# Kernel tuning notes

Hardware: AMD Instinct MI355X
Metric: run time of the kernel (lower is better)

## Reference

```python
import jax, jax.numpy as jnp
import numpy as np

D_MODEL = 1024
D_FF = 4096
N_EXPERTS = 8
THRESHOLD = 0.8
EPS = 1e-6


def setup_inputs() -> dict:
    key = jax.random.key(0)
    ks = jax.random.split(key, 8)
    x = jax.random.normal(ks[0], (2, 1024, D_MODEL), jnp.float32)
    Wg = jax.random.normal(ks[1], (D_MODEL, N_EXPERTS), jnp.float32) * (D_MODEL ** -0.5)
    bg = jnp.zeros((N_EXPERTS,), jnp.float32)
    W1 = jax.random.normal(ks[2], (N_EXPERTS, D_MODEL, D_FF), jnp.float32) * (D_MODEL ** -0.5)
    b1 = jnp.zeros((N_EXPERTS, D_FF), jnp.float32)
    W3 = jax.random.normal(ks[3], (N_EXPERTS, D_MODEL, D_FF), jnp.float32) * (D_MODEL ** -0.5)
    b3 = jnp.zeros((N_EXPERTS, D_FF), jnp.float32)
    W2 = jax.random.normal(ks[4], (N_EXPERTS, D_FF, D_MODEL), jnp.float32) * (D_FF ** -0.5)
    b2 = jnp.zeros((N_EXPERTS, D_MODEL), jnp.float32)
    return {"x": x, "Wg": Wg, "bg": bg, "W1": W1, "b1": b1, "W3": W3, "b3": b3, "W2": W2, "b2": b2}


def _route(x, Wg, bg):
    # Dynamic-K (top-p) router
    logits = x @ Wg + bg                                  # [B,S,E]
    probs = jax.nn.softmax(logits, axis=-1)
    order = jnp.argsort(-probs, axis=-1)                  # descending sort indices
    sp = jnp.take_along_axis(probs, order, axis=-1)       # sorted probs
    shifted = jnp.cumsum(sp, axis=-1) - sp                # exclusive cumsum
    active = shifted < THRESHOLD
    active = active.at[..., 0].set(True)                  # always keep top-1
    ap = sp * active.astype(sp.dtype)
    aw = ap / (ap.sum(axis=-1, keepdims=True) + EPS)      # renormalized weights
    inv = jnp.argsort(order, axis=-1)                     # scatter == gather by inverse perm
    weights = jnp.take_along_axis(aw, inv, axis=-1)       # [B,S,E] in expert order
    return weights, probs, active.sum(axis=-1)


def reference(x, Wg, bg, W1, b1, W3, b3, W2, b2):
    B, S, D = x.shape
    E = W1.shape[0]
    weights, probs, active_count = _route(x, Wg, bg)
    xf = x.reshape(-1, D)                                 # [T,D]
    wf = weights.reshape(-1, E)                           # [T,E]
    # Dense grouped SwiGLU experts; zero routing weight zeroes the contribution,
    # matching the masked gather/scatter math of the original.
    h = jnp.einsum('td,edf->etf', xf, W1) + b1[:, None, :]
    g = jax.nn.silu(h) * (jnp.einsum('td,edf->etf', xf, W3) + b3[:, None, :])
    out_e = jnp.einsum('etf,efd->etd', g, W2) + b2[:, None, :]
    final = jnp.einsum('etd,te->td', out_e, wf).reshape(B, S, D)
    # auxiliary losses
    f_i = (wf > 0).astype(x.dtype).mean(axis=0)           # fraction of tokens per expert
    P_i = probs.reshape(-1, E).mean(axis=0)               # mean router prob per expert
    loss_balance = E * jnp.sum(f_i * P_i)
    loss_entropy = (-jnp.sum(probs * jnp.log(probs + EPS), axis=-1)).mean()
    return final, loss_balance, loss_entropy, active_count
```

## Files before the change

kernel.cpp:

```cpp
#include <hip/hip_runtime.h>
#include <hip/hip_bf16.h>
#include <math.h>

#define D_MODEL 1024
#define D_FF    4096
#define N_EXP   8
#define TOKENS  2048
#define THRESH  0.8f
#define EPS_R   1e-6f

#define FINAL_SIZE (TOKENS * D_MODEL)

typedef unsigned short ushort_t;
typedef __attribute__((ext_vector_type(4))) float f32x4;
typedef __attribute__((ext_vector_type(8))) short bf16x8;
typedef __attribute__((ext_vector_type(8))) unsigned short ushort8_t;

__device__ __forceinline__ unsigned short f2bf(float f) {
    unsigned u = __builtin_bit_cast(unsigned, f);
    unsigned r = (u + 0x7FFFu + ((u >> 16) & 1u)) >> 16;
    return (unsigned short)r;
}

template <typename T>
__device__ __forceinline__ void gload16(const T* gsrc, T* ldst) {
    __builtin_amdgcn_global_load_lds((const __attribute__((address_space(1))) unsigned int*)gsrc,
                                     (__attribute__((address_space(3))) unsigned int*)ldst,
                                     16, 0, 0);
}

__global__ __launch_bounds__(256) void convert_x_kernel(const float* __restrict__ x,
                                                        ushort_t* __restrict__ xbf) {
    int i = blockIdx.x * 256 + threadIdx.x;
    const float4 v = reinterpret_cast<const float4*>(x)[i];
    ushort4 o;
    o.x = f2bf(v.x); o.y = f2bf(v.y); o.z = f2bf(v.z); o.w = f2bf(v.w);
    reinterpret_cast<ushort4*>(xbf)[i] = o;
}

__global__ __launch_bounds__(256) void wconv_kernel(const float* __restrict__ in,
                                                    ushort_t* __restrict__ out,
                                                    int K, int N) {
    __shared__ float sT[32][65];
    const int e = blockIdx.z;
    const float* src = in + (size_t)e * K * N;
    ushort_t* dst = out + (size_t)e * K * N;
    const int k0 = blockIdx.y * 32, n0 = blockIdx.x * 64;
    const int t = threadIdx.x;
    {
        const int k = t >> 3;
        const int n4 = (t & 7) * 8;
        const float* s = src + (size_t)(k0 + k) * N + n0 + n4;
        float4 a = *reinterpret_cast<const float4*>(s);
        float4 b = *reinterpret_cast<const float4*>(s + 4);
        sT[k][n4 + 0] = a.x; sT[k][n4 + 1] = a.y; sT[k][n4 + 2] = a.z; sT[k][n4 + 3] = a.w;
        sT[k][n4 + 4] = b.x; sT[k][n4 + 5] = b.y; sT[k][n4 + 6] = b.z; sT[k][n4 + 7] = b.w;
    }
    __syncthreads();
    {
        const int n = t >> 2;
        const int kg = (t & 3) * 8;
        ushort8_t o;
#pragma unroll
        for (int j = 0; j < 8; ++j) o[j] = f2bf(sT[kg + j][n]);
        *reinterpret_cast<ushort8_t*>(dst + (size_t)(n0 + n) * K + k0 + kg) = o;
    }
}

__global__ __launch_bounds__(256) void router_kernel(const float* __restrict__ x,
                                                     const float* __restrict__ Wg,
                                                     const float* __restrict__ bg,
                                                     float* __restrict__ wts,
                                                     float* __restrict__ probs,
                                                     float* __restrict__ ent,
                                                     float* __restrict__ act_out)
{
    int wave = threadIdx.x >> 6;
    int lane = threadIdx.x & 63;
    int t = blockIdx.x * 4 + wave;

    float acc[8];
#pragma unroll
    for (int e = 0; e < 8; ++e) acc[e] = 0.f;

    const float* xrow = x + (size_t)t * D_MODEL;
    for (int d = lane; d < D_MODEL; d += 64) {
        float xv = xrow[d];
        const float4* wg = reinterpret_cast<const float4*>(Wg + (size_t)d * 8);
        float4 a = wg[0], b = wg[1];
        acc[0] += xv * a.x; acc[1] += xv * a.y; acc[2] += xv * a.z; acc[3] += xv * a.w;
        acc[4] += xv * b.x; acc[5] += xv * b.y; acc[6] += xv * b.z; acc[7] += xv * b.w;
    }
#pragma unroll
    for (int e = 0; e < 8; ++e) {
#pragma unroll
        for (int off = 32; off > 0; off >>= 1) acc[e] += __shfl_xor(acc[e], off);
    }

    if (lane == 0) {
        float l[8], p[8];
        float m = -1e30f;
#pragma unroll
        for (int e = 0; e < 8; ++e) { l[e] = acc[e] + bg[e]; m = fmaxf(m, l[e]); }
        float s = 0.f;
#pragma unroll
        for (int e = 0; e < 8; ++e) { p[e] = expf(l[e] - m); s += p[e]; }
        float inv = 1.f / s;
#pragma unroll
        for (int e = 0; e < 8; ++e) p[e] *= inv;

        int idx[8]; float sp[8];
#pragma unroll
        for (int e = 0; e < 8; ++e) { idx[e] = e; sp[e] = p[e]; }
        for (int i = 0; i < 8; ++i) {
            int best = i;
            for (int j = i + 1; j < 8; ++j) if (sp[j] > sp[best]) best = j;
            float tv = sp[i]; sp[i] = sp[best]; sp[best] = tv;
            int ti = idx[i]; idx[i] = idx[best]; idx[best] = ti;
        }
        float cum = 0.f, asum = 0.f, ap[8];
        int cnt = 0;
        for (int i = 0; i < 8; ++i) {
            int active = (i == 0) || (cum < THRESH);
            cum += sp[i];
            ap[i] = active ? sp[i] : 0.f;
            asum += ap[i];
            cnt += active;
        }
        float rinv = 1.f / (asum + EPS_R);
        float w[8];
        for (int i = 0; i < 8; ++i) w[idx[i]] = ap[i] * rinv;

        float* wrow = wts + (size_t)t * 8;
        float* prow = probs + (size_t)t * 8;
        float e_sum = 0.f;
#pragma unroll
        for (int e = 0; e < 8; ++e) {
            wrow[e] = w[e];
            prow[e] = p[e];
            e_sum -= p[e] * logf(p[e] + EPS_R);
        }
        ent[t] = e_sum;
        act_out[t] = (float)cnt;
    }
}

__global__ __launch_bounds__(512) void build_lists_kernel(const float* __restrict__ wts,
                                                          int* __restrict__ tok,
                                                          int* __restrict__ pos,
                                                          int* __restrict__ cnt) {
    const int e = threadIdx.x >> 6;
    const int lane = threadIdx.x & 63;
    int base = 0;
    for (int t0 = 0; t0 < TOKENS; t0 += 64) {
        int t = t0 + lane;
        float w = wts[(size_t)t * 8 + e];
        unsigned long long mask = __ballot(w > 0.f);
        int rank = __popcll(mask & ((1ull << lane) - 1ull));
        if (w > 0.f) {
            tok[e * TOKENS + base + rank] = t;
            pos[(size_t)t * 8 + e] = base + rank;
        } else {
            pos[(size_t)t * 8 + e] = -1;
        }
        base += __popcll(mask);
    }
    if (lane == 0) cnt[e] = base;
}

__global__ __launch_bounds__(256) void loss_kernel(const float* __restrict__ wts,
                                                   const float* __restrict__ probs,
                                                   const float* __restrict__ ent,
                                                   float* __restrict__ out_scalars)
{
    int tid = threadIdx.x;
    float fsum[8], psum[8], es = 0.f;
#pragma unroll
    for (int e = 0; e < 8; ++e) { fsum[e] = 0.f; psum[e] = 0.f; }
    for (int t = tid; t < TOKENS; t += 256) {
        const float* wrow = wts + (size_t)t * 8;
        const float* prow = probs + (size_t)t * 8;
#pragma unroll
        for (int e = 0; e < 8; ++e) {
            fsum[e] += (wrow[e] > 0.f) ? 1.f : 0.f;
            psum[e] += prow[e];
        }
        es += ent[t];
    }
    __shared__ float red[256];
    __shared__ float tot[17];
    for (int q = 0; q < 17; ++q) {
        float v = (q < 8) ? fsum[q] : ((q < 16) ? psum[q - 8] : es);
        red[tid] = v; __syncthreads();
        for (int s = 128; s > 0; s >>= 1) {
            if (tid < s) red[tid] += red[tid + s];
            __syncthreads();
        }
        if (tid == 0) tot[q] = red[0];
        __syncthreads();
    }
    if (tid == 0) {
        const float invT = 1.f / (float)TOKENS;
        float lb = 0.f;
        for (int e = 0; e < 8; ++e) lb += (tot[e] * invT) * (tot[8 + e] * invT);
        out_scalars[0] = 8.f * lb;
        out_scalars[1] = tot[16] * invT;
    }
}

__global__ __launch_bounds__(256, 2) void gemm1_kernel(const ushort_t* __restrict__ xbf,
                                                       const ushort_t* __restrict__ w1t,
                                                       const ushort_t* __restrict__ w3t,
                                                       const float* __restrict__ b1,
                                                       const float* __restrict__ b3,
                                                       const int* __restrict__ tok,
                                                       const int* __restrict__ cnts,
                                                       ushort_t* __restrict__ g,
                                                       int gbase) {
    const int z = blockIdx.z;
    const int ge = gbase + z;
    const int cnt = cnts[ge];
    const int m0 = blockIdx.y * 128;
    if (m0 >= cnt) return;

    __shared__ ushort_t sA[128 * 32];
    __shared__ ushort_t sB1[64 * 32];
    __shared__ ushort_t sB3[64 * 32];

    const int tid = threadIdx.x;
    const int lane = tid & 63;
    const int wave = tid >> 6;
    const int wr = wave >> 1, wc = wave & 1;
    const int n0 = blockIdx.x * 64;

    const ushort_t* w1e = w1t + (size_t)z * D_FF * D_MODEL;
    const ushort_t* w3e = w3t + (size_t)z * D_FF * D_MODEL;

    f32x4 acc1[4][2], acc3[4][2];
#pragma unroll
    for (int i = 0; i < 4; ++i)
#pragma unroll
        for (int j = 0; j < 2; ++j) { acc1[i][j] = (f32x4)0.f; acc3[i][j] = (f32x4)0.f; }

    const int srow = tid >> 2;
    const int scol = (tid & 3) * 8;

    const ushort_t* abase[2];
#pragma unroll
    for (int r = 0; r < 2; ++r) {
        int i = m0 + srow + r * 64;
        i = (i < cnt) ? i : (cnt - 1);
        abase[r] = xbf + (size_t)tok[ge * TOKENS + i] * D_MODEL + scol;
    }

    for (int kk = 0; kk < D_MODEL; kk += 32) {
#pragma unroll
        for (int r = 0; r < 2; ++r)
            gload16(abase[r] + kk, sA + r * 2048 + wave * 512);
        gload16(w1e + (size_t)(n0 + srow) * D_MODEL + kk + scol, sB1 + wave * 512);
        gload16(w3e + (size_t)(n0 + srow) * D_MODEL + kk + scol, sB3 + wave * 512);
        __syncthreads();

        const int ko = (lane >> 4) * 8;
        bf16x8 a[4], u1[2], u3[2];
#pragma unroll
        for (int fm = 0; fm < 4; ++fm)
            a[fm] = *reinterpret_cast<const bf16x8*>(&sA[(wr * 64 + fm * 16 + (lane & 15)) * 32 + ko]);
#pragma unroll
        for (int fn = 0; fn < 2; ++fn) {
            u1[fn] = *reinterpret_cast<const bf16x8*>(&sB1[(wc * 32 + fn * 16 + (lane & 15)) * 32 + ko]);
            u3[fn] = *reinterpret_cast<const bf16x8*>(&sB3[(wc * 32 + fn * 16 + (lane & 15)) * 32 + ko]);
        }
#pragma unroll
        for (int fm = 0; fm < 4; ++fm)
#pragma unroll
            for (int fn = 0; fn < 2; ++fn) {
                acc1[fm][fn] = __builtin_amdgcn_mfma_f32_16x16x32_bf16(a[fm], u1[fn], acc1[fm][fn], 0, 0, 0);
                acc3[fm][fn] = __builtin_amdgcn_mfma_f32_16x16x32_bf16(a[fm], u3[fn], acc3[fm][fn], 0, 0, 0);
            }
        __syncthreads();
    }

    ushort_t* ge_out = g + (size_t)z * TOKENS * D_FF;
#pragma unroll
    for (int fn = 0; fn < 2; ++fn) {
        int col = n0 + wc * 32 + fn * 16 + (lane & 15);
        float bb1 = b1[(size_t)ge * D_FF + col];
        float bb3 = b3[(size_t)ge * D_FF + col];
#pragma unroll
        for (int fm = 0; fm < 4; ++fm) {
#pragma unroll
            for (int r = 0; r < 4; ++r) {
                int row = m0 + wr * 64 + fm * 16 + (lane >> 4) * 4 + r;
                if (row < cnt) {
                    float h1 = acc1[fm][fn][r] + bb1;
                    float h3 = acc3[fm][fn][r] + bb3;
                    float gv = (h1 / (1.f + expf(-h1))) * h3;
                    ge_out[(size_t)row * D_FF + col] = f2bf(gv);
                }
            }
        }
    }
}

__global__ __launch_bounds__(256, 2) void gemm2_kernel(const ushort_t* __restrict__ g,
                                                       const ushort_t* __restrict__ w2t,
                                                       const float* __restrict__ b2,
                                                       const float* __restrict__ wts,
                                                       const int* __restrict__ tok,
                                                       const int* __restrict__ cnts,
                                                       float* __restrict__ part,
                                                       int gbase) {
    const int z = blockIdx.z;
    const int ge = gbase + z;
    const int cnt = cnts[ge];
    const int m0 = blockIdx.y * 128;
    if (m0 >= cnt) return;

    __shared__ ushort_t sA[128 * 32];
    __shared__ ushort_t sB[64 * 32];

    const int tid = threadIdx.x;
    const int lane = tid & 63;
    const int wave = tid >> 6;
    const int wr = wave >> 1, wc = wave & 1;
    const int n0 = blockIdx.x * 64;

    const ushort_t* ga = g + (size_t)z * TOKENS * D_FF;
    const ushort_t* w2e = w2t + (size_t)z * D_MODEL * D_FF;

    f32x4 acc[4][2];
#pragma unroll
    for (int i = 0; i < 4; ++i)
#pragma unroll
        for (int j = 0; j < 2; ++j) acc[i][j] = (f32x4)0.f;

    const int srow = tid >> 2;
    const int scol = (tid & 3) * 8;

    for (int kk = 0; kk < D_FF; kk += 32) {
#pragma unroll
        for (int r = 0; r < 2; ++r)
            gload16(ga + (size_t)(m0 + srow + r * 64) * D_FF + kk + scol,
                    sA + r * 2048 + wave * 512);
        gload16(w2e + (size_t)(n0 + srow) * D_FF + kk + scol, sB + wave * 512);
        __syncthreads();

        const int ko = (lane >> 4) * 8;
        bf16x8 a[4], b[2];
#pragma unroll
        for (int fm = 0; fm < 4; ++fm)
            a[fm] = *reinterpret_cast<const bf16x8*>(&sA[(wr * 64 + fm * 16 + (lane & 15)) * 32 + ko]);
#pragma unroll
        for (int fn = 0; fn < 2; ++fn)
            b[fn] = *reinterpret_cast<const bf16x8*>(&sB[(wc * 32 + fn * 16 + (lane & 15)) * 32 + ko]);
#pragma unroll
        for (int fm = 0; fm < 4; ++fm)
#pragma unroll
            for (int fn = 0; fn < 2; ++fn)
                acc[fm][fn] = __builtin_amdgcn_mfma_f32_16x16x32_bf16(a[fm], b[fn], acc[fm][fn], 0, 0, 0);
        __syncthreads();
    }

    float* pe = part + (size_t)ge * TOKENS * D_MODEL;
    float bb2[2];
#pragma unroll
    for (int fn = 0; fn < 2; ++fn)
        bb2[fn] = b2[(size_t)ge * D_MODEL + n0 + wc * 32 + fn * 16 + (lane & 15)];
#pragma unroll
    for (int fm = 0; fm < 4; ++fm) {
#pragma unroll
        for (int r = 0; r < 4; ++r) {
            int row = m0 + wr * 64 + fm * 16 + (lane >> 4) * 4 + r;
            if (row < cnt) {
                float w = wts[(size_t)tok[ge * TOKENS + row] * 8 + ge];
#pragma unroll
                for (int fn = 0; fn < 2; ++fn) {
                    int col = n0 + wc * 32 + fn * 16 + (lane & 15);
                    pe[(size_t)row * D_MODEL + col] = (acc[fm][fn][r] + bb2[fn]) * w;
                }
            }
        }
    }
}

__global__ __launch_bounds__(256) void reduce_out_kernel(const float* __restrict__ part,
                                                         const int* __restrict__ pos,
                                                         float* __restrict__ out) {
    const int t = blockIdx.x;
    const int d = threadIdx.x;
    float4 s = make_float4(0.f, 0.f, 0.f, 0.f);
#pragma unroll
    for (int e = 0; e < 8; ++e) {
        int p = pos[(size_t)t * 8 + e];
        if (p >= 0) {
            float4 v = reinterpret_cast<const float4*>(part + ((size_t)e * TOKENS + p) * D_MODEL)[d];
            s.x += v.x; s.y += v.y; s.z += v.z; s.w += v.w;
        }
    }
    reinterpret_cast<float4*>(out + (size_t)t * D_MODEL)[d] = s;
}

extern "C" void kernel_launch(void* const* d_in, const int* in_sizes, int n_in,
                              void* d_out, int out_size, void* d_ws, size_t ws_size,
                              hipStream_t stream) {
    const float* x  = (const float*)d_in[0];
    const float* Wg = (const float*)d_in[1];
    const float* bg = (const float*)d_in[2];
    const float* W1 = (const float*)d_in[3];
    const float* b1 = (const float*)d_in[4];
    const float* W3 = (const float*)d_in[5];
    const float* b3 = (const float*)d_in[6];
    const float* W2 = (const float*)d_in[7];
    const float* b2 = (const float*)d_in[8];
    float* out = (float*)d_out;

    char* wsb = (char*)d_ws;
    ushort_t* xbf  = (ushort_t*)(wsb);
    float*    wts  = (float*)(wsb + (4u << 20));
    float*    probs= (float*)(wsb + (4u << 20) + 65536);
    float*    ent  = (float*)(wsb + (4u << 20) + 131072);
    int*      tok  = (int*)(wsb + (4u << 20) + 139264);
    int*      pos  = (int*)(wsb + (4u << 20) + 204800);
    int*      cnts = (int*)(wsb + (4u << 20) + 270336);
    float*    part = (float*)(wsb + (8u << 20));

    const size_t BIG0 = (size_t)72 << 20;
    const size_t PER_E = (size_t)40 << 20;
    int GS = 4;
    if (ws_size < BIG0 + 4 * PER_E) GS = 2;
    if (ws_size < BIG0 + 2 * PER_E) GS = 1;

    char* big = wsb + BIG0;
    const size_t W_SZ = (size_t)GS * ((size_t)D_FF * D_MODEL * 2);
    ushort_t* w1t  = (ushort_t*)big;
    ushort_t* w3t  = (ushort_t*)(big + W_SZ);
    ushort_t* w2t  = (ushort_t*)(big + 2 * W_SZ);
    ushort_t* gbuf = (ushort_t*)(big + 3 * W_SZ);

    float* out_scalars = out + FINAL_SIZE;
    float* out_act     = out + FINAL_SIZE + 2;

    convert_x_kernel<<<TOKENS * D_MODEL / (256 * 4), 256, 0, stream>>>(x, xbf);
    router_kernel<<<TOKENS / 4, 256, 0, stream>>>(x, Wg, bg, wts, probs, ent, out_act);
    build_lists_kernel<<<1, 512, 0, stream>>>(wts, tok, pos, cnts);
    loss_kernel<<<1, 256, 0, stream>>>(wts, probs, ent, out_scalars);

    for (int g0 = 0; g0 < N_EXP; g0 += GS) {
        wconv_kernel<<<dim3(D_FF / 64, D_MODEL / 32, GS), 256, 0, stream>>>(
            W1 + (size_t)g0 * D_MODEL * D_FF, w1t, D_MODEL, D_FF);
        wconv_kernel<<<dim3(D_FF / 64, D_MODEL / 32, GS), 256, 0, stream>>>(
            W3 + (size_t)g0 * D_MODEL * D_FF, w3t, D_MODEL, D_FF);
        wconv_kernel<<<dim3(D_MODEL / 64, D_FF / 32, GS), 256, 0, stream>>>(
            W2 + (size_t)g0 * D_FF * D_MODEL, w2t, D_FF, D_MODEL);

        gemm1_kernel<<<dim3(D_FF / 64, TOKENS / 128, GS), 256, 0, stream>>>(
            xbf, w1t, w3t, b1, b3, tok, cnts, gbuf, g0);
        gemm2_kernel<<<dim3(D_MODEL / 64, TOKENS / 128, GS), 256, 0, stream>>>(
            gbuf, w2t, b2, wts, tok, cnts, part, g0);
    }
    reduce_out_kernel<<<TOKENS, 256, 0, stream>>>(part, pos, out);
}
```

Baseline: 611.0 us.

## Double-buffer LDS tiles in both expert GEMM kernels to overlap loads with MFMA

Both grouped GEMM kernels now use ping-pong shared-memory buffers. The next K-slice is issued into the alternate buffer before the current slice is computed, and the loop is manually unrolled by two with one barrier per half-step. The goal is to hide global-to-LDS load latency behind MFMA work and to halve the number of barriers per K step. In exchange, LDS use per block doubles, which could limit occupancy at the requested two blocks per CU.

```diff
diff --git a/kernel.cpp b/kernel.cpp
--- a/kernel.cpp
+++ b/kernel.cpp
@@ -223,9 +223,9 @@
     const int m0 = blockIdx.y * 128;
     if (m0 >= cnt) return;
 
-    __shared__ ushort_t sA[128 * 32];
-    __shared__ ushort_t sB1[64 * 32];
-    __shared__ ushort_t sB3[64 * 32];
+    __shared__ ushort_t sA0[128 * 32], sA1[128 * 32];
+    __shared__ ushort_t sB10[64 * 32], sB11[64 * 32];
+    __shared__ ushort_t sB30[64 * 32], sB31[64 * 32];
 
     const int tid = threadIdx.x;
     const int lane = tid & 63;
@@ -233,9 +233,6 @@
     const int wr = wave >> 1, wc = wave & 1;
     const int n0 = blockIdx.x * 64;
 
-    const ushort_t* w1e = w1t + (size_t)z * D_FF * D_MODEL;
-    const ushort_t* w3e = w3t + (size_t)z * D_FF * D_MODEL;
-
     f32x4 acc1[4][2], acc3[4][2];
 #pragma unroll
     for (int i = 0; i < 4; ++i)
@@ -252,24 +249,25 @@
         i = (i < cnt) ? i : (cnt - 1);
         abase[r] = xbf + (size_t)tok[ge * TOKENS + i] * D_MODEL + scol;
     }
-
-    for (int kk = 0; kk < D_MODEL; kk += 32) {
-#pragma unroll
-        for (int r = 0; r < 2; ++r)
-            gload16(abase[r] + kk, sA + r * 2048 + wave * 512);
-        gload16(w1e + (size_t)(n0 + srow) * D_MODEL + kk + scol, sB1 + wave * 512);
-        gload16(w3e + (size_t)(n0 + srow) * D_MODEL + kk + scol, sB3 + wave * 512);
-        __syncthreads();
-
+    const ushort_t* w1p = w1t + (size_t)z * D_FF * D_MODEL + (size_t)(n0 + srow) * D_MODEL + scol;
+    const ushort_t* w3p = w3t + (size_t)z * D_FF * D_MODEL + (size_t)(n0 + srow) * D_MODEL + scol;
+
+    auto stage = [&](ushort_t* dA, ushort_t* dB1, ushort_t* dB3, int kk) {
+        gload16(abase[0] + kk, dA + wave * 512);
+        gload16(abase[1] + kk, dA + 2048 + wave * 512);
+        gload16(w1p + kk, dB1 + wave * 512);
+        gload16(w3p + kk, dB3 + wave * 512);
+    };
+    auto compute = [&](const ushort_t* pA, const ushort_t* pB1, const ushort_t* pB3) {
         const int ko = (lane >> 4) * 8;
         bf16x8 a[4], u1[2], u3[2];
 #pragma unroll
         for (int fm = 0; fm < 4; ++fm)
-            a[fm] = *reinterpret_cast<const bf16x8*>(&sA[(wr * 64 + fm * 16 + (lane & 15)) * 32 + ko]);
+            a[fm] = *reinterpret_cast<const bf16x8*>(&pA[(wr * 64 + fm * 16 + (lane & 15)) * 32 + ko]);
 #pragma unroll
         for (int fn = 0; fn < 2; ++fn) {
-            u1[fn] = *reinterpret_cast<const bf16x8*>(&sB1[(wc * 32 + fn * 16 + (lane & 15)) * 32 + ko]);
-            u3[fn] = *reinterpret_cast<const bf16x8*>(&sB3[(wc * 32 + fn * 16 + (lane & 15)) * 32 + ko]);
+            u1[fn] = *reinterpret_cast<const bf16x8*>(&pB1[(wc * 32 + fn * 16 + (lane & 15)) * 32 + ko]);
+            u3[fn] = *reinterpret_cast<const bf16x8*>(&pB3[(wc * 32 + fn * 16 + (lane & 15)) * 32 + ko]);
         }
 #pragma unroll
         for (int fm = 0; fm < 4; ++fm)
@@ -278,6 +276,18 @@
                 acc1[fm][fn] = __builtin_amdgcn_mfma_f32_16x16x32_bf16(a[fm], u1[fn], acc1[fm][fn], 0, 0, 0);
                 acc3[fm][fn] = __builtin_amdgcn_mfma_f32_16x16x32_bf16(a[fm], u3[fn], acc3[fm][fn], 0, 0, 0);
             }
+    };
+
+    stage(sA0, sB10, sB30, 0);
+    __syncthreads();
+
+#pragma unroll 1
+    for (int t = 0; t < 32; t += 2) {
+        if (t + 1 < 32) stage(sA1, sB11, sB31, (t + 1) * 32);
+        compute(sA0, sB10, sB30);
+        __syncthreads();
+        if (t + 2 < 32) stage(sA0, sB10, sB30, (t + 2) * 32);
+        compute(sA1, sB11, sB31);
         __syncthreads();
     }
 
@@ -317,8 +327,8 @@
     const int m0 = blockIdx.y * 128;
     if (m0 >= cnt) return;
 
-    __shared__ ushort_t sA[128 * 32];
-    __shared__ ushort_t sB[64 * 32];
+    __shared__ ushort_t sA0[128 * 32], sA1[128 * 32];
+    __shared__ ushort_t sB0[64 * 32], sB1[64 * 32];
 
     const int tid = threadIdx.x;
     const int lane = tid & 63;
@@ -326,9 +336,6 @@
     const int wr = wave >> 1, wc = wave & 1;
     const int n0 = blockIdx.x * 64;
 
-    const ushort_t* ga = g + (size_t)z * TOKENS * D_FF;
-    const ushort_t* w2e = w2t + (size_t)z * D_MODEL * D_FF;
-
     f32x4 acc[4][2];
 #pragma unroll
     for (int i = 0; i < 4; ++i)
@@ -338,27 +345,42 @@
     const int srow = tid >> 2;
     const int scol = (tid & 3) * 8;
 
-    for (int kk = 0; kk < D_FF; kk += 32) {
-#pragma unroll
-        for (int r = 0; r < 2; ++r)
-            gload16(ga + (size_t)(m0 + srow + r * 64) * D_FF + kk + scol,
-                    sA + r * 2048 + wave * 512);
-        gload16(w2e + (size_t)(n0 + srow) * D_FF + kk + scol, sB + wave * 512);
-        __syncthreads();
-
+    const ushort_t* ga = g + (size_t)z * TOKENS * D_FF;
+    const ushort_t* ap0 = ga + (size_t)(m0 + srow) * D_FF + scol;
+    const ushort_t* ap1 = ga + (size_t)(m0 + srow + 64) * D_FF + scol;
+    const ushort_t* bp  = w2t + (size_t)z * D_MODEL * D_FF + (size_t)(n0 + srow) * D_FF + scol;
+
+    auto stage = [&](ushort_t* dA, ushort_t* dB, int kk) {
+        gload16(ap0 + kk, dA + wave * 512);
+        gload16(ap1 + kk, dA + 2048 + wave * 512);
+        gload16(bp + kk, dB + wave * 512);
+    };
+    auto compute = [&](const ushort_t* pA, const ushort_t* pB) {
         const int ko = (lane >> 4) * 8;
         bf16x8 a[4], b[2];
 #pragma unroll
         for (int fm = 0; fm < 4; ++fm)
-            a[fm] = *reinterpret_cast<const bf16x8*>(&sA[(wr * 64 + fm * 16 + (lane & 15)) * 32 + ko]);
+            a[fm] = *reinterpret_cast<const bf16x8*>(&pA[(wr * 64 + fm * 16 + (lane & 15)) * 32 + ko]);
 #pragma unroll
         for (int fn = 0; fn < 2; ++fn)
-            b[fn] = *reinterpret_cast<const bf16x8*>(&sB[(wc * 32 + fn * 16 + (lane & 15)) * 32 + ko]);
+            b[fn] = *reinterpret_cast<const bf16x8*>(&pB[(wc * 32 + fn * 16 + (lane & 15)) * 32 + ko]);
 #pragma unroll
         for (int fm = 0; fm < 4; ++fm)
 #pragma unroll
             for (int fn = 0; fn < 2; ++fn)
                 acc[fm][fn] = __builtin_amdgcn_mfma_f32_16x16x32_bf16(a[fm], b[fn], acc[fm][fn], 0, 0, 0);
+    };
+
+    stage(sA0, sB0, 0);
+    __syncthreads();
+
+#pragma unroll 1
+    for (int t = 0; t < 128; t += 2) {
+        if (t + 1 < 128) stage(sA1, sB1, (t + 1) * 32);
+        compute(sA0, sB0);
+        __syncthreads();
+        if (t + 2 < 128) stage(sA0, sB0, (t + 2) * 32);
+        compute(sA1, sB1);
         __syncthreads();
     }
 
```

Result: no change. 605.6 us (-0.9%).
